# Performance work log

Hardware: AMD Instinct MI355X
Metric: run time of the kernel (lower is better)

Reference implementation:

```python
import jax, jax.numpy as jnp
import numpy as np

G, N, F, H, E = 3, 40000, 256, 128, 640000


def gcn_conv(x, W, b, edge_index):
    """PyG GCNConv: x @ W, add self-loops, sym-normalized scatter-add, + bias."""
    n = x.shape[0]
    x = x @ W
    loop = jnp.arange(n)
    row = jnp.concatenate([edge_index[0], loop])  # source nodes
    col = jnp.concatenate([edge_index[1], loop])  # target nodes
    deg = jax.ops.segment_sum(jnp.ones_like(row, dtype=x.dtype), col, num_segments=n)
    dinv = jnp.where(deg > 0, jax.lax.rsqrt(jnp.maximum(deg, 1e-12)), 0.0)
    norm = dinv[row] * dinv[col]
    out = jax.ops.segment_sum(x[row] * norm[:, None], col, num_segments=n)
    return out + b


def setup_inputs() -> dict:
    key = jax.random.key(0)
    ks = jax.random.split(key, 14)
    inp = {
        'x': jax.random.normal(ks[0], (G, N, F), jnp.float32),
        'edge_index': jax.random.randint(ks[1], (G, 2, E), 0, N, jnp.int64),
        'fc1_W': jax.random.normal(ks[2], (G, F, H), jnp.float32) * 0.05,
        'fc1_b': jax.random.normal(ks[3], (G, H), jnp.float32) * 0.05,
        'conv1_W': jax.random.normal(ks[4], (G, H, H), jnp.float32) * 0.05,
        'conv1_b': jax.random.normal(ks[5], (G, H), jnp.float32) * 0.05,
        'conv2_W': jax.random.normal(ks[6], (G, H, H), jnp.float32) * 0.05,
        'conv2_b': jax.random.normal(ks[7], (G, H), jnp.float32) * 0.05,
        'dconv1_W': jax.random.normal(ks[8], (G, H, H), jnp.float32) * 0.05,
        'dconv1_b': jax.random.normal(ks[9], (G, H), jnp.float32) * 0.05,
        'dconv2_W': jax.random.normal(ks[10], (G, H, H), jnp.float32) * 0.05,
        'dconv2_b': jax.random.normal(ks[11], (G, H), jnp.float32) * 0.05,
        'fc2_W': jax.random.normal(ks[12], (H, F), jnp.float32) * 0.05,
        'fc2_b': jax.random.normal(ks[13], (F,), jnp.float32) * 0.05,
    }
    return inp


def reference(x, edge_index, fc1_W, fc1_b, conv1_W, conv1_b, conv2_W, conv2_b,
              dconv1_W, dconv1_b, dconv2_W, dconv2_b, fc2_W, fc2_b):
    def encoder(xi, ei, fw, fb, c1w, c1b, c2w, c2b):
        pre = xi @ fw + fb                     # fc1
        h = gcn_conv(pre, c1w, c1b, ei)
        h = gcn_conv(h, c2w, c2b, ei)
        return pre, jax.nn.relu(h)

    pre_feat, enc = jax.vmap(encoder)(x, edge_index, fc1_W, fc1_b,
                                      conv1_W, conv1_b, conv2_W, conv2_b)

    # Faithful reproduction of the sequentially-mutating cross-graph block.
    h = [enc[i] for i in range(G)]
    for i in range(G):
        for j in range(G):
            if j != i:
                h[i] = h[i] + h[j]
        h[i] = h[G - 1] - h[i]  # loop var j ends at G-1 (zeroes tensor when i==G-1)
        h[i] = gcn_conv(h[i], dconv1_W[i], dconv1_b[i], edge_index[i])
        h[i] = gcn_conv(h[i], dconv2_W[i], dconv2_b[i], edge_index[i])

    fin_feat = h[0]
    for k in range(1, G - 1):
        fin_feat = fin_feat + h[k]

    loss_embedding = jax.nn.softmax(fin_feat @ fc2_W + fc2_b, axis=-1)
    return pre_feat, enc, jnp.stack(h), fin_feat, loss_embedding
```

## Files before the change

kernel.cpp:

```cpp
#include <hip/hip_runtime.h>
#include <hip/hip_bf16.h>

#define NV 40000
#define FD 256
#define HD 128
#define ED 640000
#define NG 3
#define NH (NV*HD)

#define CH  64
#define EPC (ED/CH)
#define NB  625
#define TOT (NB*CH)
#define OFFS (TOT+2)

typedef unsigned short u16;
typedef unsigned int   u32;
typedef __attribute__((ext_vector_type(8))) u16    u16x8;
typedef __attribute__((ext_vector_type(8))) __bf16 bf16x8;
typedef __attribute__((ext_vector_type(4))) float  f32x4;

__device__ inline u16 f2b(float f){ __bf16 h = (__bf16)f; return __builtin_bit_cast(u16, h); }
__device__ inline float b2f(u16 u){ u32 x = ((u32)u)<<16; return __builtin_bit_cast(float, x); }

__global__ __launch_bounds__(256) void hist_k(const int* __restrict__ ei, int* __restrict__ hist){
  int ch = blockIdx.x, g = blockIdx.y, t = threadIdx.x;
  __shared__ int h[NB];
  for (int i=t;i<NB;i+=256) h[i]=0;
  __syncthreads();
  const int* cc = ei + (long)g*2*ED + ED + ch*EPC;
  for (int j=t;j<EPC;j+=256) atomicAdd(&h[cc[j]>>6],1);
  __syncthreads();
  int* hg = hist + (long)g*TOT;
  for (int b=t;b<NB;b+=256) hg[b*CH+ch]=h[b];
}

__global__ void scan2_k(const int* __restrict__ hist, int* __restrict__ off){
  int g = blockIdx.x;
  const int* src = hist + (long)g*TOT;
  int* dst = off + (long)g*OFFS;
  __shared__ int wsum[16];
  __shared__ int carrySh;
  int tid=threadIdx.x, lane=tid&63, wv=tid>>6;
  if (tid==0) carrySh=0;
  __syncthreads();
  for (int base=0;base<TOT;base+=1024){
    int i=base+tid;
    int v=(i<TOT)?src[i]:0;
    int s=v;
    #pragma unroll
    for (int d=1;d<64;d<<=1){ int t2=__shfl_up(s,d,64); if(lane>=d) s+=t2; }
    if(lane==63) wsum[wv]=s;
    __syncthreads();
    int carry=carrySh;
    if(wv==0){
      int t3=(lane<16)?wsum[lane]:0;
      #pragma unroll
      for(int d=1;d<16;d<<=1){ int u=__shfl_up(t3,d,64); if(lane>=d) t3+=u; }
      if(lane<16) wsum[lane]=t3;
    }
    __syncthreads();
    int woff=(wv>0)?wsum[wv-1]:0;
    int incl=s+woff+carry;
    if(i<TOT){ dst[i]=incl-v; if(i==TOT-1) dst[TOT]=incl; }
    __syncthreads();
    if(tid==1023) carrySh=incl;
    __syncthreads();
  }
}

__global__ __launch_bounds__(256) void scat_k(const int* __restrict__ ei, const int* __restrict__ off,
                                              u32* __restrict__ temp){
  int ch=blockIdx.x, g=blockIdx.y, t=threadIdx.x;
  __shared__ int cur[NB];
  const int* offg = off + (long)g*OFFS;
  for (int b=t;b<NB;b+=256) cur[b]=offg[b*CH+ch];
  __syncthreads();
  const int* rr = ei + (long)g*2*ED + ch*EPC;
  const int* cc = rr + ED;
  u32* tg = temp + (long)g*ED;
  for (int j=t;j<EPC;j+=256){
    int r=rr[j], c=cc[j];
    int pos=atomicAdd(&cur[c>>6],1);
    tg[pos]=((u32)(c&63)<<16)|(u32)r;
  }
}

__global__ __launch_bounds__(256) void sort_k(const u32* __restrict__ temp, const int* __restrict__ off,
                                              u16* __restrict__ csr, int* __restrict__ cptr,
                                              float* __restrict__ dinv){
  int b=blockIdx.x, g=blockIdx.y, t=threadIdx.x;
  __shared__ int cnt[64];
  __shared__ int cur[64];
  if (t<64) cnt[t]=0;
  __syncthreads();
  const u32* tg = temp + (long)g*ED;
  const int* offg = off + (long)g*OFFS;
  int s=offg[b*CH], e=offg[(b+1)*CH];
  for (int i=s+t;i<e;i+=256) atomicAdd(&cnt[tg[i]>>16],1);
  __syncthreads();
  if (t<64){
    int v=cnt[t];
    int sc=v;
    #pragma unroll
    for (int d=1;d<64;d<<=1){ int u=__shfl_up(sc,d,64); if(t>=d) sc+=u; }
    int st = s + sc - v;
    cur[t]=st;
    cptr[(long)g*(NV+1) + b*64 + t] = st;
    if (b==NB-1 && t==63) cptr[(long)g*(NV+1)+NV] = e;
    dinv[(long)g*NV + b*64 + t] = rsqrtf((float)v+1.0f);
  }
  __syncthreads();
  u16* cg = csr + (long)g*ED;
  for (int i=s+t;i<e;i+=256){
    u32 tt=tg[i];
    int pos=atomicAdd(&cur[tt>>16],1);
    cg[pos]=(u16)(tt&0xFFFF);
  }
}

__device__ inline void tr_seg(const float* __restrict__ src, u16* __restrict__ dst,
                              int K, int NN, long idx, long total){
  if (idx>=total) return;
  long per=(long)K*NN; long mat=idx/per; long rem=idx-mat*per;
  int k=(int)(rem/NN), c=(int)(rem-(long)k*NN);
  dst[mat*per+(long)c*K+k]=f2b(src[idx]);
}

__global__ __launch_bounds__(256) void trall_k(
    const float* fc1W, const float* c1W, const float* c2W,
    const float* d1W, const float* d2W, const float* fc2W,
    u16* w_fc1, u16* w_c1, u16* w_c2, u16* w_d1, u16* w_d2, u16* w_fc2,
    const float* b1g2, const float* W2g2, float* yv)
{
  int blk=blockIdx.x, t=threadIdx.x;
  if (blk < 384)       tr_seg(fc1W, w_fc1, FD, HD, (long)blk*256+t,        (long)NG*FD*HD);
  else if (blk < 576)  tr_seg(c1W,  w_c1,  HD, HD, (long)(blk-384)*256+t,  (long)NG*HD*HD);
  else if (blk < 768)  tr_seg(c2W,  w_c2,  HD, HD, (long)(blk-576)*256+t,  (long)NG*HD*HD);
  else if (blk < 960)  tr_seg(d1W,  w_d1,  HD, HD, (long)(blk-768)*256+t,  (long)NG*HD*HD);
  else if (blk < 1152) tr_seg(d2W,  w_d2,  HD, HD, (long)(blk-960)*256+t,  (long)NG*HD*HD);
  else if (blk < 1280) tr_seg(fc2W, w_fc2, HD, FD, (long)(blk-1152)*256+t, (long)HD*FD);
  else if (t < HD){
    float s=0.f;
    for (int k=0;k<HD;k++) s += b1g2[k]*W2g2[(long)k*HD+t];
    yv[t]=s;
  }
}

template<int MODE>
__global__ __launch_bounds__(256) void gemm_k(
    const void* __restrict__ A_, const void* __restrict__ A2_, long sA,
    const u16* __restrict__ Bt, long sB,
    const float* __restrict__ bias, long sBias,
    const float* __restrict__ scale, long sSc,
    float* __restrict__ Cf, long sCf,
    u16* __restrict__ Cb, long sCb,
    int M, int N, int K)
{
  __shared__ __align__(16) u16 lsA[128*64];
  __shared__ __align__(16) u16 lsB[128*64];
  const int gz = blockIdx.z;
  const float* Af  = (const float*)A_  + (long)gz*sA;
  const float* Af2 = (const float*)A2_ + (long)gz*sA;
  const u16*   Ab  = (const u16*)  A_  + (long)gz*sA;
  const u16* Bp = Bt + (long)gz*sB;
  const int t = threadIdx.x;
  const int lane = t & 63, wv = t >> 6, wm = wv >> 1, wn = wv & 1;
  const int lr = lane & 15, lq = lane >> 4;
  const int ar = t >> 1, ah = t & 1;
  const long grow = (long)blockIdx.x*128 + ar;
  const int colB = blockIdx.y*128 + ar;

  f32x4 acc[4][4];
  #pragma unroll
  for (int m=0;m<4;m++)
    #pragma unroll
    for (int n=0;n<4;n++) acc[m][n] = (f32x4)(0.0f);

  for (int k0=0; k0<K; k0+=64){
    if (k0) __syncthreads();
    u16x8 av[4];
    if (grow < M){
      if (MODE==0){
        const u16x8* s = (const u16x8*)(Ab + grow*(long)K + k0 + ah*32);
        #pragma unroll
        for (int i=0;i<4;i++) av[i] = s[i];
      } else if (MODE==1){
        const float4* s = (const float4*)(Af + grow*(long)K + k0 + ah*32);
        #pragma unroll
        for (int i=0;i<4;i++){
          float4 v0 = s[i*2], v1 = s[i*2+1];
          u16x8 w;
          w[0]=f2b(v0.x); w[1]=f2b(v0.y); w[2]=f2b(v0.z); w[3]=f2b(v0.w);
          w[4]=f2b(v1.x); w[5]=f2b(v1.y); w[6]=f2b(v1.z); w[7]=f2b(v1.w);
          av[i] = w;
        }
      } else {
        const float4* s0 = (const float4*)(Af  + grow*(long)K + k0 + ah*32);
        const float4* s1 = (const float4*)(Af2 + grow*(long)K + k0 + ah*32);
        #pragma unroll
        for (int i=0;i<4;i++){
          float4 a0 = s0[i*2], a1 = s0[i*2+1];
          float4 b0 = s1[i*2], b1 = s1[i*2+1];
          float x0,x1,x2,x3,y0,y1,y2,y3;
          if (MODE==2){
            x0=-(a0.x+b0.x); x1=-(a0.y+b0.y); x2=-(a0.z+b0.z); x3=-(a0.w+b0.w);
            y0=-(a1.x+b1.x); y1=-(a1.y+b1.y); y2=-(a1.z+b1.z); y3=-(a1.w+b1.w);
          } else {
            x0=a0.x+b0.x; x1=a0.y+b0.y; x2=a0.z+b0.z; x3=a0.w+b0.w;
            y0=a1.x+b1.x; y1=a1.y+b1.y; y2=a1.z+b1.z; y3=a1.w+b1.w;
          }
          u16x8 w;
          w[0]=f2b(x0); w[1]=f2b(x1); w[2]=f2b(x2); w[3]=f2b(x3);
          w[4]=f2b(y0); w[5]=f2b(y1); w[6]=f2b(y2); w[7]=f2b(y3);
          av[i] = w;
        }
      }
    } else {
      #pragma unroll
      for (int i=0;i<4;i++) av[i] = (u16x8)((u16)0);
    }
    #pragma unroll
    for (int i=0;i<4;i++){
      int q = ah*4 + i;
      *(u16x8*)&lsA[ar*64 + ((q ^ (ar&7))<<3)] = av[i];
    }
    {
      const u16x8* s = (const u16x8*)(Bp + (long)colB*K + k0 + ah*32);
      #pragma unroll
      for (int i=0;i<4;i++){
        int q = ah*4 + i;
        *(u16x8*)&lsB[ar*64 + ((q ^ (ar&7))<<3)] = s[i];
      }
    }
    __syncthreads();
    #pragma unroll
    for (int kk=0; kk<2; kk++){
      bf16x8 afr[4], bfr[4];
      #pragma unroll
      for (int m=0;m<4;m++){
        int r = wm*64 + m*16 + lr;
        int q = kk*4 + lq;
        afr[m] = __builtin_bit_cast(bf16x8, *(const u16x8*)&lsA[r*64 + ((q ^ (r&7))<<3)]);
      }
      #pragma unroll
      for (int n=0;n<4;n++){
        int r = wn*64 + n*16 + lr;
        int q = kk*4 + lq;
        bfr[n] = __builtin_bit_cast(bf16x8, *(const u16x8*)&lsB[r*64 + ((q ^ (r&7))<<3)]);
      }
      #pragma unroll
      for (int m=0;m<4;m++)
        #pragma unroll
        for (int n=0;n<4;n++)
          acc[m][n] = __builtin_amdgcn_mfma_f32_16x16x32_bf16(afr[m], bfr[n], acc[m][n], 0, 0, 0);
    }
  }
  #pragma unroll
  for (int m=0;m<4;m++){
    long gr0 = (long)blockIdx.x*128 + wm*64 + m*16 + lq*4;
    #pragma unroll
    for (int n=0;n<4;n++){
      int gc = blockIdx.y*128 + wn*64 + n*16 + lr;
      float bb = bias ? bias[gz*sBias + gc] : 0.0f;
      #pragma unroll
      for (int i=0;i<4;i++){
        long gr = gr0 + i;
        if (gr < M){
          float v = acc[m][n][i] + bb;
          if (Cf) Cf[gz*sCf + gr*(long)N + gc] = v;
          if (Cb){
            float sc = scale ? scale[gz*sSc + gr] : 1.0f;
            Cb[gz*sCb + gr*(long)N + gc] = f2b(v*sc);
          }
        }
      }
    }
  }
}

__global__ __launch_bounds__(256) void agg3_k(
    const u16* __restrict__ xw, long sXW,
    const u16* __restrict__ csr, long sCsr,
    const int* __restrict__ cptr, long sCp,
    const float* __restrict__ dinv, long sD,
    const float* __restrict__ bias, long sBias,
    float* __restrict__ outF, long sOF,
    u16* __restrict__ outB, long sOB,
    int totWaves, int relu)
{
  int wid = (int)((blockIdx.x*256 + threadIdx.x) >> 6);
  if (wid >= totWaves) return;
  int lane = threadIdx.x & 63;
  int g = wid / NV;
  int c = wid - g*NV;
  const u32* xp = (const u32*)(xw + (long)g*sXW);
  const u16* cg = csr + (long)g*sCsr;
  const int* cp = cptr + (long)g*sCp;
  float dc = dinv[(long)g*sD + c];
  u32 u = xp[(long)c*64 + lane];
  float sx = b2f((u16)u), sy = b2f((u16)(u>>16));
  int j0 = cp[c], j1 = cp[c+1];
  int deg = j1 - j0;
  int idx = 0;
  if (lane < deg) idx = cg[j0 + lane];
  int kmax = min(deg, 64);
  int k = 0;
  for (; k+4<=kmax; k+=4){
    int r0=__shfl(idx,k,64), r1=__shfl(idx,k+1,64), r2=__shfl(idx,k+2,64), r3=__shfl(idx,k+3,64);
    u32 v0=xp[(long)r0*64+lane], v1=xp[(long)r1*64+lane];
    u32 v2=xp[(long)r2*64+lane], v3=xp[(long)r3*64+lane];
    sx += b2f((u16)v0); sy += b2f((u16)(v0>>16));
    sx += b2f((u16)v1); sy += b2f((u16)(v1>>16));
    sx += b2f((u16)v2); sy += b2f((u16)(v2>>16));
    sx += b2f((u16)v3); sy += b2f((u16)(v3>>16));
  }
  for (; k<kmax; ++k){
    int r=__shfl(idx,k,64);
    u32 v=xp[(long)r*64+lane];
    sx += b2f((u16)v); sy += b2f((u16)(v>>16));
  }
  for (int j=j0+64; j<j1; ++j){
    int r=cg[j];
    u32 v=xp[(long)r*64+lane];
    sx += b2f((u16)v); sy += b2f((u16)(v>>16));
  }
  float ox = dc*sx + bias[g*sBias + lane*2];
  float oy = dc*sy + bias[g*sBias + lane*2 + 1];
  if (relu){ ox=fmaxf(ox,0.f); oy=fmaxf(oy,0.f); }
  if (outF) ((float2*)(outF + (long)g*sOF + (long)c*HD))[lane] = make_float2(ox, oy);
  if (outB) ((u32*)(outB + (long)g*sOB))[(long)c*64 + lane] = (u32)f2b(ox) | ((u32)f2b(oy)<<16);
}

__global__ __launch_bounds__(64) void h2_k(const u32* __restrict__ temp, const int* __restrict__ off,
                                           const float* __restrict__ dinv, const float* __restrict__ y,
                                           const float* __restrict__ b2, float* __restrict__ outF){
  int b=blockIdx.x, lane=threadIdx.x;
  __shared__ float sacc[64];
  sacc[lane]=0.f;
  __syncthreads();
  int s=off[b*CH], e=off[(b+1)*CH];
  for(int i=s+lane;i<e;i+=64){
    u32 t=temp[i];
    unsafeAtomicAdd(&sacc[t>>16], dinv[t&0xFFFF]);
  }
  __syncthreads();
  float y0=y[2*lane], y1=y[2*lane+1], bb0=b2[2*lane], bb1=b2[2*lane+1];
  for(int n=0;n<64;n++){
    int c=b*64+n;
    float dc=dinv[c];
    float f=dc*dc+dc*sacc[n];
    ((float2*)(outF+(long)c*HD))[lane]=make_float2(y0*f+bb0, y1*f+bb1);
  }
}

__global__ void ew_add(const float4* __restrict__ a, const float4* __restrict__ b,
                       float4* __restrict__ of, int n4){
  int i = blockIdx.x*256 + threadIdx.x;
  if (i >= n4) return;
  float4 va = a[i], vb = b[i];
  of[i] = make_float4(va.x+vb.x, va.y+vb.y, va.z+vb.z, va.w+vb.w);
}

__global__ void softmax_k(float* __restrict__ d, int rows){
  int wid = (blockIdx.x*256 + threadIdx.x) >> 6;
  if (wid >= rows) return;
  int lane = threadIdx.x & 63;
  float4* p = (float4*)(d + (long)wid*FD);
  float4 v = p[lane];
  float m = fmaxf(fmaxf(v.x, v.y), fmaxf(v.z, v.w));
  #pragma unroll
  for (int o=32; o; o>>=1) m = fmaxf(m, __shfl_xor(m, o, 64));
  float e0 = __expf(v.x-m), e1 = __expf(v.y-m), e2 = __expf(v.z-m), e3 = __expf(v.w-m);
  float s = e0+e1+e2+e3;
  #pragma unroll
  for (int o=32; o; o>>=1) s += __shfl_xor(s, o, 64);
  float inv = 1.0f/s;
  p[lane] = make_float4(e0*inv, e1*inv, e2*inv, e3*inv);
}

extern "C" void kernel_launch(void* const* d_in, const int* in_sizes, int n_in,
                              void* d_out, int out_size, void* d_ws, size_t ws_size,
                              hipStream_t stream)
{
  const float* x    = (const float*)d_in[0];
  const int*   ei   = (const int*)  d_in[1];
  const float* fc1W = (const float*)d_in[2];
  const float* fc1b = (const float*)d_in[3];
  const float* c1W  = (const float*)d_in[4];
  const float* c1b  = (const float*)d_in[5];
  const float* c2W  = (const float*)d_in[6];
  const float* c2b  = (const float*)d_in[7];
  const float* d1W  = (const float*)d_in[8];
  const float* d1b  = (const float*)d_in[9];
  const float* d2W  = (const float*)d_in[10];
  const float* d2b  = (const float*)d_in[11];
  const float* fc2W = (const float*)d_in[12];
  const float* fc2b = (const float*)d_in[13];
  (void)in_sizes; (void)n_in; (void)out_size; (void)ws_size;

  float* out  = (float*)d_out;
  float* O_pre = out;
  float* O_enc = out + (long)NG*NH;
  float* O_h   = out + 2L*NG*NH;
  float* O_fin = out + 3L*NG*NH;
  float* O_ls  = O_fin + NH;

  char* p = (char*)d_ws;
  auto alloc = [&](size_t bytes)->void*{
    void* r = (void*)p; p += (bytes + 255) & ~(size_t)255; return r;
  };
  u16* bfA    = (u16*)alloc((size_t)NG*NH*2);
  u16* bfXW   = (u16*)alloc((size_t)NG*NH*2);
  u16* wt_fc1 = (u16*)alloc((size_t)NG*FD*HD*2);
  u16* wt_c1  = (u16*)alloc((size_t)NG*HD*HD*2);
  u16* wt_c2  = (u16*)alloc((size_t)NG*HD*HD*2);
  u16* wt_d1  = (u16*)alloc((size_t)NG*HD*HD*2);
  u16* wt_d2  = (u16*)alloc((size_t)NG*HD*HD*2);
  u16* wt_fc2 = (u16*)alloc((size_t)HD*FD*2);
  u32*  temp  = (u32*) alloc((size_t)NG*ED*4);
  u16*  csr   = (u16*) alloc((size_t)NG*ED*2);
  int*  cptr  = (int*) alloc((size_t)NG*(NV+1)*4);
  int*  hist  = (int*) alloc((size_t)NG*TOT*4);
  int*  off   = (int*) alloc((size_t)NG*OFFS*4);
  float* dinv = (float*)alloc((size_t)NG*NV*4);
  float* yv   = (float*)alloc((size_t)HD*4);

  hist_k<<<dim3(CH,NG), 256, 0, stream>>>(ei, hist);
  scan2_k<<<NG, 1024, 0, stream>>>(hist, off);
  scat_k<<<dim3(CH,NG), 256, 0, stream>>>(ei, off, temp);
  sort_k<<<dim3(NB,NG), 256, 0, stream>>>(temp, off, csr, cptr, dinv);

  trall_k<<<1281, 256, 0, stream>>>(fc1W, c1W, c2W, d1W, d2W, fc2W,
                                    wt_fc1, wt_c1, wt_c2, wt_d1, wt_d2, wt_fc2,
                                    d1b + 2*HD, d2W + 2L*HD*HD, yv);

  dim3 gB((NV+127)/128, 1, NG);
  dim3 g1((NV+127)/128, 1, 1);
  dim3 g2((NV+127)/128, 2, 1);

  gemm_k<1><<<gB, 256, 0, stream>>>(x, nullptr, (long)NV*FD, wt_fc1, (long)FD*HD, fc1b, HD,
                                    nullptr, 0, O_pre, NH, bfA, NH, NV, HD, FD);
  gemm_k<0><<<gB, 256, 0, stream>>>(bfA, nullptr, NH, wt_c1, (long)HD*HD, nullptr, 0,
                                    dinv, NV, nullptr, 0, bfXW, NH, NV, HD, HD);
  agg3_k<<<NG*NV/4, 256, 0, stream>>>(bfXW, NH, csr, ED, cptr, NV+1, dinv, NV,
                                      c1b, HD, nullptr, 0, bfA, NH, NG*NV, 0);
  gemm_k<0><<<gB, 256, 0, stream>>>(bfA, nullptr, NH, wt_c2, (long)HD*HD, nullptr, 0,
                                    dinv, NV, nullptr, 0, bfXW, NH, NV, HD, HD);
  agg3_k<<<NG*NV/4, 256, 0, stream>>>(bfXW, NH, csr, ED, cptr, NV+1, dinv, NV,
                                      c2b, HD, O_enc, NH, nullptr, 0, NG*NV, 1);

  h2_k<<<NB, 64, 0, stream>>>(temp + 2L*ED, off + 2L*OFFS, dinv + 2L*NV, yv,
                              d2b + 2*HD, O_h + 2L*NH);

  for (int i=0; i<2; i++){
    const float* P0 = (i==0) ? O_enc        : (O_enc + NH);
    const float* P1 = (i==0) ? (O_enc + NH) : O_h;
    gemm_k<2><<<g1, 256, 0, stream>>>(P0, P1, 0, wt_d1 + (long)i*HD*HD, 0, nullptr, 0,
                                      dinv + (long)i*NV, 0, nullptr, 0, bfXW, 0, NV, HD, HD);
    agg3_k<<<NV/4, 256, 0, stream>>>(bfXW, 0, csr + (long)i*ED, 0, cptr + (long)i*(NV+1), 0,
                                     dinv + (long)i*NV, 0, d1b + i*HD, 0,
                                     nullptr, 0, bfA, 0, NV, 0);
    gemm_k<0><<<g1, 256, 0, stream>>>(bfA, nullptr, 0, wt_d2 + (long)i*HD*HD, 0, nullptr, 0,
                                      dinv + (long)i*NV, 0, nullptr, 0, bfXW, 0, NV, HD, HD);
    agg3_k<<<NV/4, 256, 0, stream>>>(bfXW, 0, csr + (long)i*ED, 0, cptr + (long)i*(NV+1), 0,
                                     dinv + (long)i*NV, 0, d2b + i*HD, 0,
                                     O_h + (long)i*NH, 0, nullptr, 0, NV, 0);
  }

  ew_add<<<NH/4/256, 256, 0, stream>>>((const float4*)O_h, (const float4*)(O_h+NH),
                                       (float4*)O_fin, NH/4);
  gemm_k<3><<<g2, 256, 0, stream>>>(O_h, O_h + NH, 0, wt_fc2, 0, fc2b, 0,
                                    nullptr, 0, O_ls, 0, nullptr, 0, NV, FD, HD);
  softmax_k<<<NV/4, 256, 0, stream>>>(O_ls, NV);
}
```

Measured before the change: 722.8 us.

## Fuse consecutive GCN layers algebraically: aggregate twice then one combined GEMM

Measured after the change: 603.7 us. -16.5%, faster.

```diff
diff --git a/kernel.cpp b/kernel.cpp
--- a/kernel.cpp
+++ b/kernel.cpp
@@ -11,8 +11,6 @@
 #define CH  64
 #define EPC (ED/CH)
 #define NB  625
-#define TOT (NB*CH)
-#define OFFS (TOT+2)
 
 typedef unsigned short u16;
 typedef unsigned int   u32;
@@ -23,61 +21,57 @@
 __device__ inline u16 f2b(float f){ __bf16 h = (__bf16)f; return __builtin_bit_cast(u16, h); }
 __device__ inline float b2f(u16 u){ u32 x = ((u32)u)<<16; return __builtin_bit_cast(float, x); }
 
-__global__ __launch_bounds__(256) void hist_k(const int* __restrict__ ei, int* __restrict__ hist){
-  int ch = blockIdx.x, g = blockIdx.y, t = threadIdx.x;
+__global__ __launch_bounds__(256) void histB_k(const int* __restrict__ ei, int* __restrict__ btot){
+  int ch=blockIdx.x, g=blockIdx.y, t=threadIdx.x;
   __shared__ int h[NB];
   for (int i=t;i<NB;i+=256) h[i]=0;
   __syncthreads();
   const int* cc = ei + (long)g*2*ED + ED + ch*EPC;
   for (int j=t;j<EPC;j+=256) atomicAdd(&h[cc[j]>>6],1);
   __syncthreads();
-  int* hg = hist + (long)g*TOT;
-  for (int b=t;b<NB;b+=256) hg[b*CH+ch]=h[b];
-}
-
-__global__ void scan2_k(const int* __restrict__ hist, int* __restrict__ off){
-  int g = blockIdx.x;
-  const int* src = hist + (long)g*TOT;
-  int* dst = off + (long)g*OFFS;
+  for (int b=t;b<NB;b+=256){ int v=h[b]; if(v) atomicAdd(&btot[g*NB+b], v); }
+}
+
+__global__ void scanB_k(const int* __restrict__ btot, int* __restrict__ base, int* __restrict__ gcur){
   __shared__ int wsum[16];
-  __shared__ int carrySh;
   int tid=threadIdx.x, lane=tid&63, wv=tid>>6;
-  if (tid==0) carrySh=0;
-  __syncthreads();
-  for (int base=0;base<TOT;base+=1024){
-    int i=base+tid;
-    int v=(i<TOT)?src[i]:0;
+  for (int g=0; g<NG; ++g){
+    int v = (tid<NB)? btot[g*NB+tid] : 0;
     int s=v;
     #pragma unroll
-    for (int d=1;d<64;d<<=1){ int t2=__shfl_up(s,d,64); if(lane>=d) s+=t2; }
-    if(lane==63) wsum[wv]=s;
+    for (int d=1; d<64; d<<=1){ int u=__shfl_up(s,d,64); if(lane>=d) s+=u; }
+    if (lane==63) wsum[wv]=s;
     __syncthreads();
-    int carry=carrySh;
-    if(wv==0){
+    if (wv==0){
       int t3=(lane<16)?wsum[lane]:0;
       #pragma unroll
-      for(int d=1;d<16;d<<=1){ int u=__shfl_up(t3,d,64); if(lane>=d) t3+=u; }
-      if(lane<16) wsum[lane]=t3;
+      for (int d=1; d<16; d<<=1){ int u=__shfl_up(t3,d,64); if(lane>=d) t3+=u; }
+      if (lane<16) wsum[lane]=t3;
     }
     __syncthreads();
-    int woff=(wv>0)?wsum[wv-1]:0;
-    int incl=s+woff+carry;
-    if(i<TOT){ dst[i]=incl-v; if(i==TOT-1) dst[TOT]=incl; }
+    int incl = s + (wv>0? wsum[wv-1]:0);
+    if (tid<NB){
+      base[g*(NB+1)+tid]=incl-v;
+      gcur[g*NB+tid]=incl-v;
+      if (tid==NB-1) base[g*(NB+1)+NB]=incl;
+    }
     __syncthreads();
-    if(tid==1023) carrySh=incl;
-    __syncthreads();
-  }
-}
-
-__global__ __launch_bounds__(256) void scat_k(const int* __restrict__ ei, const int* __restrict__ off,
+  }
+}
+
+__global__ __launch_bounds__(256) void scat_k(const int* __restrict__ ei, int* __restrict__ gcur,
                                               u32* __restrict__ temp){
   int ch=blockIdx.x, g=blockIdx.y, t=threadIdx.x;
+  __shared__ int h[NB];
   __shared__ int cur[NB];
-  const int* offg = off + (long)g*OFFS;
-  for (int b=t;b<NB;b+=256) cur[b]=offg[b*CH+ch];
+  for (int i=t;i<NB;i+=256) h[i]=0;
   __syncthreads();
   const int* rr = ei + (long)g*2*ED + ch*EPC;
   const int* cc = rr + ED;
+  for (int j=t;j<EPC;j+=256) atomicAdd(&h[cc[j]>>6],1);
+  __syncthreads();
+  for (int b=t;b<NB;b+=256){ int v=h[b]; cur[b] = v? atomicAdd(&gcur[g*NB+b], v) : 0; }
+  __syncthreads();
   u32* tg = temp + (long)g*ED;
   for (int j=t;j<EPC;j+=256){
     int r=rr[j], c=cc[j];
@@ -86,7 +80,7 @@
   }
 }
 
-__global__ __launch_bounds__(256) void sort_k(const u32* __restrict__ temp, const int* __restrict__ off,
+__global__ __launch_bounds__(256) void sort_k(const u32* __restrict__ temp, const int* __restrict__ base,
                                               u16* __restrict__ csr, int* __restrict__ cptr,
                                               float* __restrict__ dinv){
   int b=blockIdx.x, g=blockIdx.y, t=threadIdx.x;
@@ -95,8 +89,7 @@
   if (t<64) cnt[t]=0;
   __syncthreads();
   const u32* tg = temp + (long)g*ED;
-  const int* offg = off + (long)g*OFFS;
-  int s=offg[b*CH], e=offg[(b+1)*CH];
+  int s=base[g*(NB+1)+b], e=base[g*(NB+1)+b+1];
   for (int i=s+t;i<e;i+=256) atomicAdd(&cnt[tg[i]>>16],1);
   __syncthreads();
   if (t<64){
@@ -119,6 +112,24 @@
   }
 }
 
+__global__ __launch_bounds__(256) void svec_k(const u16* __restrict__ csr, const int* __restrict__ cptr,
+                                              const float* __restrict__ dinv, float* __restrict__ sv,
+                                              int totWaves){
+  int wid=(int)((blockIdx.x*256+threadIdx.x)>>6);
+  if (wid>=totWaves) return;
+  int lane=threadIdx.x&63;
+  int g=wid/NV, c=wid-g*NV;
+  const u16* cg=csr+(long)g*ED;
+  const int* cp=cptr+(long)g*(NV+1);
+  const float* dv=dinv+(long)g*NV;
+  int j0=cp[c], j1=cp[c+1];
+  float sum=0.f;
+  for (int j=j0+lane;j<j1;j+=64) sum+=dv[cg[j]];
+  #pragma unroll
+  for (int o=32;o;o>>=1) sum+=__shfl_xor(sum,o,64);
+  if (lane==0){ float dc=dv[c]; sv[(long)g*NV+c]=dc*(dc+sum); }
+}
+
 __device__ inline void tr_seg(const float* __restrict__ src, u16* __restrict__ dst,
                               int K, int NN, long idx, long total){
   if (idx>=total) return;
@@ -128,41 +139,60 @@
 }
 
 __global__ __launch_bounds__(256) void trall_k(
-    const float* fc1W, const float* c1W, const float* c2W,
-    const float* d1W, const float* d2W, const float* fc2W,
-    u16* w_fc1, u16* w_c1, u16* w_c2, u16* w_d1, u16* w_d2, u16* w_fc2,
-    const float* b1g2, const float* W2g2, float* yv)
+    const float* fc1W, const float* fc2W,
+    const float* c1W, const float* c2W, const float* c1b,
+    const float* d1W, const float* d2W, const float* d1b,
+    u16* w_fc1, u16* w_fc2, u16* w_ce, u16* w_cd,
+    float* t_enc, float* t_dec)
 {
   int blk=blockIdx.x, t=threadIdx.x;
-  if (blk < 384)       tr_seg(fc1W, w_fc1, FD, HD, (long)blk*256+t,        (long)NG*FD*HD);
-  else if (blk < 576)  tr_seg(c1W,  w_c1,  HD, HD, (long)(blk-384)*256+t,  (long)NG*HD*HD);
-  else if (blk < 768)  tr_seg(c2W,  w_c2,  HD, HD, (long)(blk-576)*256+t,  (long)NG*HD*HD);
-  else if (blk < 960)  tr_seg(d1W,  w_d1,  HD, HD, (long)(blk-768)*256+t,  (long)NG*HD*HD);
-  else if (blk < 1152) tr_seg(d2W,  w_d2,  HD, HD, (long)(blk-960)*256+t,  (long)NG*HD*HD);
-  else if (blk < 1280) tr_seg(fc2W, w_fc2, HD, FD, (long)(blk-1152)*256+t, (long)HD*FD);
-  else if (t < HD){
+  if (blk < 384){
+    tr_seg(fc1W, w_fc1, FD, HD, (long)blk*256+t, (long)NG*FD*HD);
+  } else if (blk < 512){
+    tr_seg(fc2W, w_fc2, HD, FD, (long)(blk-384)*256+t, (long)HD*FD);
+  } else if (blk < 832){
+    int bb=blk-512;
+    int mat=bb>>6;
+    int local=(bb&63)*256+t;
+    int n=local>>7, k=local&127;
+    const float* W1; const float* W2; u16* dst;
+    if (mat<3){ W1=c1W+(long)mat*HD*HD; W2=c2W+(long)mat*HD*HD; dst=w_ce+(long)mat*HD*HD; }
+    else { int md=mat-3; W1=d1W+(long)md*HD*HD; W2=d2W+(long)md*HD*HD; dst=w_cd+(long)md*HD*HD; }
     float s=0.f;
-    for (int k=0;k<HD;k++) s += b1g2[k]*W2g2[(long)k*HD+t];
-    yv[t]=s;
-  }
-}
-
-template<int MODE>
+    for (int j=0;j<HD;j++) s += W1[k*HD+j]*W2[j*HD+n];
+    dst[(long)n*HD+k]=f2b(s);
+  } else {
+    for (int idx=t; idx<768; idx+=256){
+      int which=idx>>7, n=idx&127;
+      const float* b; const float* W; float* dst;
+      if (which<3){ b=c1b+which*HD; W=c2W+(long)which*HD*HD; dst=t_enc+which*HD; }
+      else { int w2=which-3; b=d1b+w2*HD; W=d2W+(long)w2*HD*HD; dst=t_dec+w2*HD; }
+      float s=0.f;
+      for (int k=0;k<HD;k++) s += b[k]*W[(long)k*HD+n];
+      dst[n]=s;
+    }
+  }
+}
+
+template<int MODE, int EX>
 __global__ __launch_bounds__(256) void gemm_k(
-    const void* __restrict__ A_, const void* __restrict__ A2_, long sA,
+    const void* __restrict__ A_, long sA,
     const u16* __restrict__ Bt, long sB,
-    const float* __restrict__ bias, long sBias,
-    const float* __restrict__ scale, long sSc,
+    const float* __restrict__ biasCol, long sBias,
+    const float* __restrict__ svec, long sS,
+    const float* __restrict__ tvec,
+    const float* __restrict__ scaleRow, long sSc,
+    const float* __restrict__ Add,
     float* __restrict__ Cf, long sCf,
+    float* __restrict__ Cf2,
     u16* __restrict__ Cb, long sCb,
-    int M, int N, int K)
+    int M, int N, int K, int relu)
 {
   __shared__ __align__(16) u16 lsA[128*64];
   __shared__ __align__(16) u16 lsB[128*64];
   const int gz = blockIdx.z;
-  const float* Af  = (const float*)A_  + (long)gz*sA;
-  const float* Af2 = (const float*)A2_ + (long)gz*sA;
-  const u16*   Ab  = (const u16*)  A_  + (long)gz*sA;
+  const float* Af = (const float*)A_ + (long)gz*sA;
+  const u16*   Ab = (const u16*)  A_ + (long)gz*sA;
   const u16* Bp = Bt + (long)gz*sB;
   const int t = threadIdx.x;
   const int lane = t & 63, wv = t >> 6, wm = wv >> 1, wn = wv & 1;
@@ -185,7 +215,7 @@
         const u16x8* s = (const u16x8*)(Ab + grow*(long)K + k0 + ah*32);
         #pragma unroll
         for (int i=0;i<4;i++) av[i] = s[i];
-      } else if (MODE==1){
+      } else {
         const float4* s = (const float4*)(Af + grow*(long)K + k0 + ah*32);
         #pragma unroll
         for (int i=0;i<4;i++){
@@ -195,26 +225,6 @@
           w[4]=f2b(v1.x); w[5]=f2b(v1.y); w[6]=f2b(v1.z); w[7]=f2b(v1.w);
           av[i] = w;
         }
-      } else {
-        const float4* s0 = (const float4*)(Af  + grow*(long)K + k0 + ah*32);
-        const float4* s1 = (const float4*)(Af2 + grow*(long)K + k0 + ah*32);
-        #pragma unroll
-        for (int i=0;i<4;i++){
-          float4 a0 = s0[i*2], a1 = s0[i*2+1];
-          float4 b0 = s1[i*2], b1 = s1[i*2+1];
-          float x0,x1,x2,x3,y0,y1,y2,y3;
-          if (MODE==2){
-            x0=-(a0.x+b0.x); x1=-(a0.y+b0.y); x2=-(a0.z+b0.z); x3=-(a0.w+b0.w);
-            y0=-(a1.x+b1.x); y1=-(a1.y+b1.y); y2=-(a1.z+b1.z); y3=-(a1.w+b1.w);
-          } else {
-            x0=a0.x+b0.x; x1=a0.y+b0.y; x2=a0.z+b0.z; x3=a0.w+b0.w;
-            y0=a1.x+b1.x; y1=a1.y+b1.y; y2=a1.z+b1.z; y3=a1.w+b1.w;
-          }
-          u16x8 w;
-          w[0]=f2b(x0); w[1]=f2b(x1); w[2]=f2b(x2); w[3]=f2b(x3);
-          w[4]=f2b(y0); w[5]=f2b(y1); w[6]=f2b(y2); w[7]=f2b(y3);
-          av[i] = w;
-        }
       }
     } else {
       #pragma unroll
@@ -262,16 +272,28 @@
     #pragma unroll
     for (int n=0;n<4;n++){
       int gc = blockIdx.y*128 + wn*64 + n*16 + lr;
-      float bb = bias ? bias[gz*sBias + gc] : 0.0f;
+      float bb = biasCol[gz*sBias + gc];
+      float tv = (svec!=nullptr) ? tvec[gz*sBias + gc] : 0.0f;
       #pragma unroll
       for (int i=0;i<4;i++){
         long gr = gr0 + i;
         if (gr < M){
           float v = acc[m][n][i] + bb;
-          if (Cf) Cf[gz*sCf + gr*(long)N + gc] = v;
-          if (Cb){
-            float sc = scale ? scale[gz*sSc + gr] : 1.0f;
-            Cb[gz*sCb + gr*(long)N + gc] = f2b(v*sc);
+          if (svec!=nullptr) v += svec[gz*sS + gr]*tv;
+          if (relu) v = fmaxf(v, 0.0f);
+          if (EX==0){
+            if (Cf) Cf[gz*sCf + gr*(long)N + gc] = v;
+            if (Cb){
+              float sc = scaleRow ? scaleRow[gz*sSc + gr] : 1.0f;
+              Cb[gz*sCb + gr*(long)N + gc] = f2b(v*sc);
+            }
+          } else if (EX==1){
+            Cf[gz*sCf + gr*(long)N + gc] = v;
+            float z = -(v + Add[gr*(long)N + gc]) * scaleRow[gr];
+            Cb[gz*sCb + gr*(long)N + gc] = f2b(z);
+          } else {
+            Cf[gz*sCf + gr*(long)N + gc] = v;
+            Cf2[gr*(long)N + gc] = v + Add[gr*(long)N + gc];
           }
         }
       }
@@ -279,15 +301,13 @@
   }
 }
 
-__global__ __launch_bounds__(256) void agg3_k(
+__global__ __launch_bounds__(256) void agg_k(
     const u16* __restrict__ xw, long sXW,
     const u16* __restrict__ csr, long sCsr,
     const int* __restrict__ cptr, long sCp,
     const float* __restrict__ dinv, long sD,
-    const float* __restrict__ bias, long sBias,
-    float* __restrict__ outF, long sOF,
     u16* __restrict__ outB, long sOB,
-    int totWaves, int relu)
+    int totWaves, int scOut)
 {
   int wid = (int)((blockIdx.x*256 + threadIdx.x) >> 6);
   if (wid >= totWaves) return;
@@ -325,41 +345,32 @@
     u32 v=xp[(long)r*64+lane];
     sx += b2f((u16)v); sy += b2f((u16)(v>>16));
   }
-  float ox = dc*sx + bias[g*sBias + lane*2];
-  float oy = dc*sy + bias[g*sBias + lane*2 + 1];
-  if (relu){ ox=fmaxf(ox,0.f); oy=fmaxf(oy,0.f); }
-  if (outF) ((float2*)(outF + (long)g*sOF + (long)c*HD))[lane] = make_float2(ox, oy);
-  if (outB) ((u32*)(outB + (long)g*sOB))[(long)c*64 + lane] = (u32)f2b(ox) | ((u32)f2b(oy)<<16);
-}
-
-__global__ __launch_bounds__(64) void h2_k(const u32* __restrict__ temp, const int* __restrict__ off,
-                                           const float* __restrict__ dinv, const float* __restrict__ y,
-                                           const float* __restrict__ b2, float* __restrict__ outF){
-  int b=blockIdx.x, lane=threadIdx.x;
-  __shared__ float sacc[64];
-  sacc[lane]=0.f;
-  __syncthreads();
-  int s=off[b*CH], e=off[(b+1)*CH];
-  for(int i=s+lane;i<e;i+=64){
-    u32 t=temp[i];
-    unsafeAtomicAdd(&sacc[t>>16], dinv[t&0xFFFF]);
-  }
-  __syncthreads();
-  float y0=y[2*lane], y1=y[2*lane+1], bb0=b2[2*lane], bb1=b2[2*lane+1];
-  for(int n=0;n<64;n++){
-    int c=b*64+n;
-    float dc=dinv[c];
-    float f=dc*dc+dc*sacc[n];
-    ((float2*)(outF+(long)c*HD))[lane]=make_float2(y0*f+bb0, y1*f+bb1);
-  }
-}
-
-__global__ void ew_add(const float4* __restrict__ a, const float4* __restrict__ b,
-                       float4* __restrict__ of, int n4){
+  float m = scOut ? dc*dc : dc;
+  float ox = m*sx, oy = m*sy;
+  ((u32*)(outB + (long)g*sOB))[(long)c*64 + lane] = (u32)f2b(ox) | ((u32)f2b(oy)<<16);
+}
+
+__global__ void ewz_k(const float4* __restrict__ e0, const float4* __restrict__ e1,
+                      const float* __restrict__ dinv0, u16* __restrict__ outB){
   int i = blockIdx.x*256 + threadIdx.x;
-  if (i >= n4) return;
-  float4 va = a[i], vb = b[i];
-  of[i] = make_float4(va.x+vb.x, va.y+vb.y, va.z+vb.z, va.w+vb.w);
+  if (i >= NH/4) return;
+  int row = i>>5;
+  float d = dinv0[row];
+  float4 a = e0[i], b = e1[i];
+  float x0=-d*(a.x+b.x), x1=-d*(a.y+b.y), x2=-d*(a.z+b.z), x3=-d*(a.w+b.w);
+  ((uint2*)outB)[i] = make_uint2((u32)f2b(x0) | ((u32)f2b(x1)<<16),
+                                 (u32)f2b(x2) | ((u32)f2b(x3)<<16));
+}
+
+__global__ void h2_k(const float* __restrict__ sv2, const float* __restrict__ t2,
+                     const float* __restrict__ b2, float4* __restrict__ outF){
+  int i = blockIdx.x*256 + threadIdx.x;
+  if (i >= NH/4) return;
+  int row = i>>5, c4 = i&31;
+  float s = sv2[row];
+  float4 tv = ((const float4*)t2)[c4];
+  float4 bb = ((const float4*)b2)[c4];
+  outF[i] = make_float4(s*tv.x+bb.x, s*tv.y+bb.y, s*tv.z+bb.z, s*tv.w+bb.w);
 }
 
 __global__ void softmax_k(float* __restrict__ d, int rows){
@@ -411,66 +422,63 @@
     void* r = (void*)p; p += (bytes + 255) & ~(size_t)255; return r;
   };
   u16* bfA    = (u16*)alloc((size_t)NG*NH*2);
-  u16* bfXW   = (u16*)alloc((size_t)NG*NH*2);
+  u16* bfB    = (u16*)alloc((size_t)NG*NH*2);
+  u16* bfC    = (u16*)alloc((size_t)NG*NH*2);
   u16* wt_fc1 = (u16*)alloc((size_t)NG*FD*HD*2);
-  u16* wt_c1  = (u16*)alloc((size_t)NG*HD*HD*2);
-  u16* wt_c2  = (u16*)alloc((size_t)NG*HD*HD*2);
-  u16* wt_d1  = (u16*)alloc((size_t)NG*HD*HD*2);
-  u16* wt_d2  = (u16*)alloc((size_t)NG*HD*HD*2);
   u16* wt_fc2 = (u16*)alloc((size_t)HD*FD*2);
+  u16* wt_ce  = (u16*)alloc((size_t)NG*HD*HD*2);
+  u16* wt_cd  = (u16*)alloc((size_t)2*HD*HD*2);
+  float* t_enc = (float*)alloc((size_t)NG*HD*4);
+  float* t_dec = (float*)alloc((size_t)NG*HD*4);
   u32*  temp  = (u32*) alloc((size_t)NG*ED*4);
   u16*  csr   = (u16*) alloc((size_t)NG*ED*2);
   int*  cptr  = (int*) alloc((size_t)NG*(NV+1)*4);
-  int*  hist  = (int*) alloc((size_t)NG*TOT*4);
-  int*  off   = (int*) alloc((size_t)NG*OFFS*4);
+  int*  btot  = (int*) alloc((size_t)NG*NB*4);
+  int*  base  = (int*) alloc((size_t)NG*(NB+1)*4);
+  int*  gcur  = (int*) alloc((size_t)NG*NB*4);
   float* dinv = (float*)alloc((size_t)NG*NV*4);
-  float* yv   = (float*)alloc((size_t)HD*4);
-
-  hist_k<<<dim3(CH,NG), 256, 0, stream>>>(ei, hist);
-  scan2_k<<<NG, 1024, 0, stream>>>(hist, off);
-  scat_k<<<dim3(CH,NG), 256, 0, stream>>>(ei, off, temp);
-  sort_k<<<dim3(NB,NG), 256, 0, stream>>>(temp, off, csr, cptr, dinv);
-
-  trall_k<<<1281, 256, 0, stream>>>(fc1W, c1W, c2W, d1W, d2W, fc2W,
-                                    wt_fc1, wt_c1, wt_c2, wt_d1, wt_d2, wt_fc2,
-                                    d1b + 2*HD, d2W + 2L*HD*HD, yv);
-
-  dim3 gB((NV+127)/128, 1, NG);
+  float* svec = (float*)alloc((size_t)NG*NV*4);
+
+  hipMemsetAsync(btot, 0, (size_t)NG*NB*4, stream);
+  histB_k<<<dim3(CH,NG), 256, 0, stream>>>(ei, btot);
+  scanB_k<<<1, 1024, 0, stream>>>(btot, base, gcur);
+  scat_k<<<dim3(CH,NG), 256, 0, stream>>>(ei, gcur, temp);
+  sort_k<<<dim3(NB,NG), 256, 0, stream>>>(temp, base, csr, cptr, dinv);
+  svec_k<<<NG*NV/4, 256, 0, stream>>>(csr, cptr, dinv, svec, NG*NV);
+
+  trall_k<<<833, 256, 0, stream>>>(fc1W, fc2W, c1W, c2W, c1b, d1W, d2W, d1b,
+                                   wt_fc1, wt_fc2, wt_ce, wt_cd, t_enc, t_dec);
+
+  dim3 g3((NV+127)/128, 1, NG);
   dim3 g1((NV+127)/128, 1, 1);
-  dim3 g2((NV+127)/128, 2, 1);
-
-  gemm_k<1><<<gB, 256, 0, stream>>>(x, nullptr, (long)NV*FD, wt_fc1, (long)FD*HD, fc1b, HD,
-                                    nullptr, 0, O_pre, NH, bfA, NH, NV, HD, FD);
-  gemm_k<0><<<gB, 256, 0, stream>>>(bfA, nullptr, NH, wt_c1, (long)HD*HD, nullptr, 0,
-                                    dinv, NV, nullptr, 0, bfXW, NH, NV, HD, HD);
-  agg3_k<<<NG*NV/4, 256, 0, stream>>>(bfXW, NH, csr, ED, cptr, NV+1, dinv, NV,
-                                      c1b, HD, nullptr, 0, bfA, NH, NG*NV, 0);
-  gemm_k<0><<<gB, 256, 0, stream>>>(bfA, nullptr, NH, wt_c2, (long)HD*HD, nullptr, 0,
-                                    dinv, NV, nullptr, 0, bfXW, NH, NV, HD, HD);
-  agg3_k<<<NG*NV/4, 256, 0, stream>>>(bfXW, NH, csr, ED, cptr, NV+1, dinv, NV,
-                                      c2b, HD, O_enc, NH, nullptr, 0, NG*NV, 1);
-
-  h2_k<<<NB, 64, 0, stream>>>(temp + 2L*ED, off + 2L*OFFS, dinv + 2L*NV, yv,
-                              d2b + 2*HD, O_h + 2L*NH);
-
-  for (int i=0; i<2; i++){
-    const float* P0 = (i==0) ? O_enc        : (O_enc + NH);
-    const float* P1 = (i==0) ? (O_enc + NH) : O_h;
-    gemm_k<2><<<g1, 256, 0, stream>>>(P0, P1, 0, wt_d1 + (long)i*HD*HD, 0, nullptr, 0,
-                                      dinv + (long)i*NV, 0, nullptr, 0, bfXW, 0, NV, HD, HD);
-    agg3_k<<<NV/4, 256, 0, stream>>>(bfXW, 0, csr + (long)i*ED, 0, cptr + (long)i*(NV+1), 0,
-                                     dinv + (long)i*NV, 0, d1b + i*HD, 0,
-                                     nullptr, 0, bfA, 0, NV, 0);
-    gemm_k<0><<<g1, 256, 0, stream>>>(bfA, nullptr, 0, wt_d2 + (long)i*HD*HD, 0, nullptr, 0,
-                                      dinv + (long)i*NV, 0, nullptr, 0, bfXW, 0, NV, HD, HD);
-    agg3_k<<<NV/4, 256, 0, stream>>>(bfXW, 0, csr + (long)i*ED, 0, cptr + (long)i*(NV+1), 0,
-                                     dinv + (long)i*NV, 0, d2b + i*HD, 0,
-                                     O_h + (long)i*NH, 0, nullptr, 0, NV, 0);
-  }
-
-  ew_add<<<NH/4/256, 256, 0, stream>>>((const float4*)O_h, (const float4*)(O_h+NH),
-                                       (float4*)O_fin, NH/4);
-  gemm_k<3><<<g2, 256, 0, stream>>>(O_h, O_h + NH, 0, wt_fc2, 0, fc2b, 0,
-                                    nullptr, 0, O_ls, 0, nullptr, 0, NV, FD, HD);
+  dim3 gf((NV+127)/128, 2, 1);
+
+  gemm_k<1,0><<<g3, 256, 0, stream>>>(x, (long)NV*FD, wt_fc1, (long)FD*HD, fc1b, HD,
+                                      nullptr, 0, nullptr, dinv, NV, nullptr,
+                                      O_pre, NH, nullptr, bfA, NH, NV, HD, FD, 0);
+  agg_k<<<NG*NV/4, 256, 0, stream>>>(bfA, NH, csr, ED, cptr, NV+1, dinv, NV, bfB, NH, NG*NV, 1);
+  agg_k<<<NG*NV/4, 256, 0, stream>>>(bfB, NH, csr, ED, cptr, NV+1, dinv, NV, bfC, NH, NG*NV, 0);
+  gemm_k<0,0><<<g3, 256, 0, stream>>>(bfC, NH, wt_ce, (long)HD*HD, c2b, HD,
+                                      svec, NV, t_enc, nullptr, 0, nullptr,
+                                      O_enc, NH, nullptr, nullptr, 0, NV, HD, HD, 1);
+
+  h2_k<<<NH/4/256, 256, 0, stream>>>(svec + 2L*NV, t_dec + 2*HD, d2b + 2*HD, (float4*)(O_h + 2L*NH));
+
+  ewz_k<<<NH/4/256, 256, 0, stream>>>((const float4*)O_enc, (const float4*)(O_enc+NH), dinv, bfA);
+  agg_k<<<NV/4, 256, 0, stream>>>(bfA, 0, csr, 0, cptr, 0, dinv, 0, bfB, 0, NV, 1);
+  agg_k<<<NV/4, 256, 0, stream>>>(bfB, 0, csr, 0, cptr, 0, dinv, 0, bfC, 0, NV, 0);
+  gemm_k<0,1><<<g1, 256, 0, stream>>>(bfC, 0, wt_cd, 0, d2b, 0,
+                                      svec, 0, t_dec, dinv + NV, 0, O_enc + NH,
+                                      O_h, 0, nullptr, bfA, 0, NV, HD, HD, 0);
+
+  agg_k<<<NV/4, 256, 0, stream>>>(bfA, 0, csr + (long)ED, 0, cptr + (NV+1), 0, dinv + NV, 0, bfB, 0, NV, 1);
+  agg_k<<<NV/4, 256, 0, stream>>>(bfB, 0, csr + (long)ED, 0, cptr + (NV+1), 0, dinv + NV, 0, bfC, 0, NV, 0);
+  gemm_k<0,2><<<g1, 256, 0, stream>>>(bfC, 0, wt_cd + (long)HD*HD, 0, d2b + HD, 0,
+                                      svec + NV, 0, t_dec + HD, nullptr, 0, O_h,
+                                      O_h + NH, 0, O_fin, nullptr, 0, NV, HD, HD, 0);
+
+  gemm_k<1,0><<<gf, 256, 0, stream>>>(O_fin, 0, wt_fc2, 0, fc2b, 0,
+                                      nullptr, 0, nullptr, nullptr, 0, nullptr,
+                                      O_ls, 0, nullptr, nullptr, 0, NV, FD, HD, 0);
   softmax_k<<<NV/4, 256, 0, stream>>>(O_ls, NV);
 }
```
